# Optimization experiments

Hardware: AMD Instinct MI355X
Metric: run time of the kernel (lower is better)

The kernel has to match this reference:

```python
import jax, jax.numpy as jnp
import numpy as np

NG, NP = 40000, 80000
E = 150000
HID = 256; OUT = 256; H = 4; L = 2
D = HID // H  # 64
IN_G, IN_P = 128, 64
EDGE_DEFS = [(0, 1), (1, 0), (1, 1)]  # (src_type, dst_type): gene->peak, peak->gene, peak->peak
SCALE = 1.0 / float(np.sqrt(D))


def setup_inputs():
    key = jax.random.key(0)
    ks = iter(jax.random.split(key, 64))
    def nrm(shape, s=0.05):
        return jax.random.normal(next(ks), shape, dtype=jnp.float32) * s
    inp = {}
    inp['x_gene'] = jax.random.normal(next(ks), (NG, IN_G), dtype=jnp.float32)
    inp['x_peak'] = jax.random.normal(next(ks), (NP, IN_P), dtype=jnp.float32)
    def edges(ns, nd):
        return jnp.stack([jax.random.randint(next(ks), (E,), 0, ns),
                          jax.random.randint(next(ks), (E,), 0, nd)])
    inp['ei_gp'] = edges(NG, NP)
    inp['ei_pg'] = edges(NP, NG)
    inp['ei_pp'] = edges(NP, NP)
    # input projections per node type
    inp['W_in_g'] = nrm((IN_G, HID)); inp['b_in_g'] = jnp.zeros((HID,), jnp.float32)
    inp['W_in_p'] = nrm((IN_P, HID)); inp['b_in_p'] = jnp.zeros((HID,), jnp.float32)
    # HGTConv params, stacked over [layer, node_type] or [layer, edge_type]
    inp['Wk'] = nrm((L, 2, HID, HID)); inp['bk'] = jnp.zeros((L, 2, HID), jnp.float32)
    inp['Wq'] = nrm((L, 2, HID, HID)); inp['bq'] = jnp.zeros((L, 2, HID), jnp.float32)
    inp['Wv'] = nrm((L, 2, HID, HID)); inp['bv'] = jnp.zeros((L, 2, HID), jnp.float32)
    inp['a_rel'] = nrm((L, 3, H, D, D), 0.1)  # per-edge-type key transform
    inp['m_rel'] = nrm((L, 3, H, D, D), 0.1)  # per-edge-type message transform
    inp['p_rel'] = jnp.ones((L, 3, H), jnp.float32)  # relation prior
    inp['W_oc'] = nrm((L, 2, HID, HID)); inp['b_oc'] = jnp.zeros((L, 2, HID), jnp.float32)
    inp['skip'] = jnp.zeros((L, 2), jnp.float32)  # per-node-type skip logits
    # output projections per node type
    inp['W_out_g'] = nrm((HID, OUT)); inp['b_out_g'] = jnp.zeros((OUT,), jnp.float32)
    inp['W_out_p'] = nrm((HID, OUT)); inp['b_out_p'] = jnp.zeros((OUT,), jnp.float32)
    return inp


def _hgt_conv(xs, eis, Wk, bk, Wq, bq, Wv, bv, a_rel, m_rel, p_rel, W_oc, b_oc, skip):
    # xs: list of [N_t, HID] per node type; eis: list of [2, E] per edge type
    k = [(xs[t] @ Wk[t] + bk[t]).reshape(-1, H, D) for t in range(2)]
    q = [(xs[t] @ Wq[t] + bq[t]).reshape(-1, H, D) for t in range(2)]
    v = [(xs[t] @ Wv[t] + bv[t]).reshape(-1, H, D) for t in range(2)]
    logits = [[], []]; msgs = [[], []]; dsts = [[], []]
    for r, (st, dt) in enumerate(EDGE_DEFS):
        src, dst = eis[r][0], eis[r][1]
        k_t = jnp.einsum('nhd,hdf->nhf', k[st], a_rel[r])  # relation-specific keys at node level
        v_t = jnp.einsum('nhd,hdf->nhf', v[st], m_rel[r])  # relation-specific messages
        lg = jnp.einsum('ehd,ehd->eh', k_t[src], q[dt][dst]) * p_rel[r] * SCALE  # [E, H]
        logits[dt].append(lg); msgs[dt].append(v_t[src]); dsts[dt].append(dst)
    out = []
    for t in range(2):
        n = xs[t].shape[0]
        lg = jnp.concatenate(logits[t]); ms = jnp.concatenate(msgs[t]); dd = jnp.concatenate(dsts[t])
        # segment softmax over all incoming edges (across edge types) per dst node
        mx = jax.ops.segment_max(lg, dd, num_segments=n)            # [n, H]
        ex = jnp.exp(lg - mx[dd])
        den = jax.ops.segment_sum(ex, dd, num_segments=n)
        alpha = ex / den[dd]                                        # [Etot, H]
        agg = jax.ops.segment_sum(alpha[:, :, None] * ms, dd, num_segments=n).reshape(n, HID)
        o = jax.nn.gelu(agg) @ W_oc[t] + b_oc[t]
        a = jax.nn.sigmoid(skip[t])
        out.append(a * o + (1.0 - a) * xs[t])
    return out


def reference(x_gene, x_peak, ei_gp, ei_pg, ei_pp, W_in_g, b_in_g, W_in_p, b_in_p,
              Wk, bk, Wq, bq, Wv, bv, a_rel, m_rel, p_rel, W_oc, b_oc, skip,
              W_out_g, b_out_g, W_out_p, b_out_p):
    # eval mode: dropout disabled
    xs = [jax.nn.relu(x_gene @ W_in_g + b_in_g), jax.nn.relu(x_peak @ W_in_p + b_in_p)]
    eis = [ei_gp, ei_pg, ei_pp]
    for l in range(L):
        xs = _hgt_conv(xs, eis, Wk[l], bk[l], Wq[l], bq[l], Wv[l], bv[l],
                       a_rel[l], m_rel[l], p_rel[l], W_oc[l], b_oc[l], skip[l])
        xs = [jax.nn.relu(x) for x in xs]
    z_g = xs[0] @ W_out_g + b_out_g
    z_p = xs[1] @ W_out_p + b_out_p
    return z_g, z_p
```

## Files before the change

### kernel.cpp

```cpp
#include <hip/hip_runtime.h>

typedef unsigned short u16;
typedef unsigned int u32;
typedef __bf16 bf16x8 __attribute__((ext_vector_type(8)));
typedef float f32x4 __attribute__((ext_vector_type(4)));

#define AS_G __attribute__((address_space(1)))
#define AS_L __attribute__((address_space(3)))

__device__ __forceinline__ float b2f(u16 u){ union{u32 i; float f;}x; x.i=((u32)u)<<16; return x.f; }
__device__ __forceinline__ u16 f2b(float f){ union{float f; u32 i;}x; x.f=f; u32 r=(x.i+0x7FFFu+((x.i>>16)&1u))>>16; return (u16)r; }

__global__ void fill_f32(float* __restrict__ p, int n, float v){
  int i = blockIdx.x * 256 + threadIdx.x;
  if (i < n) p[i] = v;
}
__global__ void diag_f32(const int* __restrict__ flag, float* __restrict__ p, int n){
  if (flag[0] == 0) return;
  for (int i = blockIdx.x * 256 + threadIdx.x; i < n; i += gridDim.x * 256) p[i] = 3.0f;
}
__global__ void detect_k(const int* __restrict__ ei, int* __restrict__ mode){
  if (threadIdx.x == 0 && blockIdx.x == 0)
    mode[0] = ((ei[1] | ei[3] | ei[5] | ei[7]) == 0) ? 1 : 0;
}

__global__ void scatter_k(const int* __restrict__ ei_gp, const int* __restrict__ ei_pg,
                          const int* __restrict__ ei_pp, int E,
                          const int* __restrict__ mode,
                          int* __restrict__ cntg, int* __restrict__ cntp,
                          u32* __restrict__ slg, u32* __restrict__ slp,
                          int* __restrict__ flag)
{
  const u32 PBASE = 40000u * 768u;
  int e = blockIdx.x * 256 + threadIdx.x;
  if (e >= E) return;
  int y = blockIdx.y;
  const int* ei = (y == 0) ? ei_pg : (y == 1) ? ei_gp : ei_pp;
  int nsrc      = (y == 1) ? 40000 : 80000;
  int ndst      = (y == 0) ? 40000 : 80000;
  int* cnt      = (y == 0) ? cntg : cntp;
  u32* slots    = (y == 0) ? slg  : slp;
  int src, dst;
  if (mode[0]){ src = ei[2*(size_t)e]; dst = ei[2*(size_t)E + 2*(size_t)e]; }
  else        { src = ei[e];           dst = ei[(size_t)E + e]; }
  if ((u32)src >= (u32)nsrc || (u32)dst >= (u32)ndst){ atomicOr(flag, 1); return; }
  u32 off, rel;
  if (y == 1){ off = (u32)src * 768u + 256u;          rel = 0u; }
  else if (y == 0){ off = PBASE + (u32)src * 1280u + 256u; rel = 1u; }
  else            { off = PBASE + (u32)src * 1280u + 768u; rel = 2u; }
  int slot = atomicAdd(&cnt[dst], 1);
  if (slot < 32) slots[(size_t)dst * 32 + slot] = off | (rel << 28);
}

struct GP {
  const u16* A; int lda;
  const u16* Bt;
  const float* bias;
  const u16* xres;
  const float* skipp;
  void* C; int ldc;
  int M, K, N;
};

template<int EPI, int F32OUT>
__global__ __launch_bounds__(512)
void gemm_bt(GP p0, GP p1)
{
  const GP P = blockIdx.z ? p1 : p0;
  __shared__ __align__(16) u16 smem[24576];
  u16* Al = smem;
  u16* Bl = smem + 16384;
  const int tid  = threadIdx.x;
  const int lane = tid & 63;
  const int wid  = tid >> 6;
  const int wr   = wid >> 1, wc = wid & 1;

  const int NC = gridDim.x, NR = gridDim.y;
  const int f  = blockIdx.y * NC + blockIdx.x;
  const int NR8 = NR & ~7;
  int c, r;
  const int bulk = NC * NR8;
  if (f < bulk){
    int xcd = f & 7;
    int j = f >> 3;
    c = j % NC;
    r = (j / NC) * 8 + xcd;
  } else {
    int f2 = f - bulk;
    c = f2 % NC;
    r = NR8 + f2 / NC;
  }
  const int row0 = r * 256, col0 = c * 128;
  if (row0 >= P.M || col0 >= P.N) return;

  f32x4 acc[4][4] = {};
  const int cr  = tid >> 3;
  const int ccs = (((tid & 7) ^ (cr & 7)) * 8);

  for (int k0 = 0; k0 < P.K; k0 += 64){
    #pragma unroll
    for (int i = 0; i < 4; i++){
      int grow = row0 + i*64 + cr; grow = grow < P.M ? grow : (P.M - 1);
      const u16* g = P.A + (size_t)grow * P.lda + (k0 + ccs);
      u16* l = Al + i*4096 + wid*512;
      __builtin_amdgcn_global_load_lds((const AS_G void*)g, (AS_L void*)l, 16, 0, 0);
    }
    #pragma unroll
    for (int i = 0; i < 2; i++){
      const u16* g = P.Bt + (size_t)(col0 + i*64 + cr) * P.K + (k0 + ccs);
      u16* l = Bl + i*4096 + wid*512;
      __builtin_amdgcn_global_load_lds((const AS_G void*)g, (AS_L void*)l, 16, 0, 0);
    }
    __syncthreads();
    #pragma unroll
    for (int ks = 0; ks < 2; ks++){
      bf16x8 aF[4], bF[4];
      const int ch8 = (((ks*4 + (lane >> 4)) ^ (lane & 7))) * 8;
      #pragma unroll
      for (int m = 0; m < 4; m++)
        aF[m] = *(const bf16x8*)&Al[(size_t)(wr*64 + m*16 + (lane & 15)) * 64 + ch8];
      #pragma unroll
      for (int n = 0; n < 4; n++)
        bF[n] = *(const bf16x8*)&Bl[(size_t)(wc*64 + n*16 + (lane & 15)) * 64 + ch8];
      #pragma unroll
      for (int m = 0; m < 4; m++)
        #pragma unroll
        for (int n = 0; n < 4; n++)
          acc[m][n] = __builtin_amdgcn_mfma_f32_16x16x32_bf16(aF[m], bF[n], acc[m][n], 0, 0, 0);
    }
    __syncthreads();
  }

  float ask = 0.f;
  if (EPI == 2) ask = 1.f / (1.f + __expf(-(*P.skipp)));

  if (F32OUT){
    #pragma unroll
    for (int n = 0; n < 4; n++){
      const int col = col0 + wc*64 + n*16 + (lane & 15);
      const float bv = P.bias[col];
      #pragma unroll
      for (int m = 0; m < 4; m++){
        const int rb = row0 + wr*64 + m*16 + (lane >> 4) * 4;
        #pragma unroll
        for (int j = 0; j < 4; j++){
          int row = rb + j;
          if (row < P.M) ((float*)P.C)[(size_t)row*P.ldc + col] = acc[m][n][j] + bv;
        }
      }
    }
  } else {
    #pragma unroll
    for (int chh = 0; chh < 2; chh++){
      __syncthreads();
      if (wc == chh){
        #pragma unroll
        for (int n = 0; n < 4; n++){
          const int cl = n*16 + (lane & 15);
          const int col = col0 + chh*64 + cl;
          const float bv = P.bias[col];
          #pragma unroll
          for (int m = 0; m < 4; m++){
            const int rlb = wr*64 + m*16 + (lane >> 4) * 4;
            #pragma unroll
            for (int j = 0; j < 4; j++){
              const int rl = rlb + j;
              float v = acc[m][n][j] + bv;
              if (EPI == 1) v = fmaxf(v, 0.f);
              if (EPI == 2){
                int row = row0 + rl;
                float xr = (row < P.M) ? b2f(P.xres[(size_t)row*256 + col]) : 0.f;
                v = ask * v + (1.f - ask) * xr;
                v = fmaxf(v, 0.f);
              }
              smem[rl*72 + cl] = f2b(v);
            }
          }
        }
      }
      __syncthreads();
      #pragma unroll
      for (int t = 0; t < 4; t++){
        int idx = t*512 + tid;
        int rr2 = idx >> 3, cchunk = idx & 7;
        int grow = row0 + rr2;
        if (grow < P.M)
          *(bf16x8*)((u16*)P.C + (size_t)grow*P.ldc + col0 + chh*64 + cchunk*8) =
              *(const bf16x8*)&smem[rr2*72 + cchunk*8];
      }
    }
  }
}

__global__ void cvt_k(const float* __restrict__ in, u16* __restrict__ out, int n4){
  int i = blockIdx.x * 256 + threadIdx.x;
  if (i >= n4) return;
  float4 v = ((const float4*)in)[i];
  u16 o[4] = { f2b(v.x), f2b(v.y), f2b(v.z), f2b(v.w) };
  *(unsigned long long*)&out[(size_t)i*4] = *(unsigned long long*)o;
}

__global__ void transpose_k(const float* __restrict__ W, u16* __restrict__ Wt, int K, int N){
  int idx = blockIdx.x * 256 + threadIdx.x;
  if (idx >= K * N) return;
  int n = idx / K, k = idx % K;
  Wt[idx] = f2b(W[(size_t)k * N + n]);
}
__global__ void transpose10_k(const float* __restrict__ Wq, const float* __restrict__ Woc,
                              const float* __restrict__ Wog, const float* __restrict__ Wop,
                              u16* __restrict__ wqkv_g, u16* __restrict__ wqkv_p,
                              u16* __restrict__ woct, u16* __restrict__ woutt)
{
  int y = blockIdx.y;
  const float* W; u16* D;
  if (y < 4){ int l = y >> 1, t = y & 1;
              W = Wq + (size_t)y*65536;
              D = t ? (wqkv_p + (size_t)l*1280*256) : (wqkv_g + (size_t)l*768*256); }
  else if (y < 8){ W = Woc + (size_t)(y-4)*65536; D = woct + (size_t)(y-4)*65536; }
  else if (y == 8){ W = Wog; D = woutt; }
  else            { W = Wop; D = woutt + 65536; }
  int idx = blockIdx.x * 256 + threadIdx.x;
  int n = idx >> 8, k = idx & 255;
  D[(size_t)n*256 + k] = f2b(W[(size_t)k*256 + n]);
}

__global__ void fuse_rel_k(const float* __restrict__ Wk, const float* __restrict__ Wv,
                           const float* __restrict__ a_rel, const float* __restrict__ m_rel,
                           u16* __restrict__ wqkv_g, u16* __restrict__ wqkv_p)
{
  int y = blockIdx.y;
  int l = y / 6, rr = y % 6, rel = rr >> 1, kv = rr & 1;
  int st = (rel == 0) ? 0 : 1;
  const float* W    = (kv ? Wv : Wk) + (size_t)l*131072 + (size_t)st*65536;
  const float* arel = (kv ? m_rel : a_rel) + (size_t)l*49152 + (size_t)rel*16384;
  u16* base; size_t ld; int rowoff;
  if (rel == 0){ base = wqkv_g; ld = 768;  rowoff = 256 + kv*256; }
  else if (rel == 1){ base = wqkv_p; ld = 1280; rowoff = 256 + kv*256; }
  else              { base = wqkv_p; ld = 1280; rowoff = 768 + kv*256; }
  u16* dst = base + (size_t)l*ld*256 + (size_t)rowoff*256;
  int fo = threadIdx.x;
  int c  = blockIdx.x;
  int h = fo >> 6, f = fo & 63;
  const float* wrow = W + (size_t)c*256 + h*64;
  const float* arow = arel + (size_t)h*4096 + f;
  float s = 0.f;
  #pragma unroll 8
  for (int d = 0; d < 64; d++) s += wrow[d] * arow[(size_t)d*64];
  dst[(size_t)fo*256 + c] = f2b(s);
}

__global__ void fuse_bias_k(const float* __restrict__ bk, const float* __restrict__ bv,
                            const float* __restrict__ bq,
                            const float* __restrict__ a_rel, const float* __restrict__ m_rel,
                            float* __restrict__ bqkv_g, float* __restrict__ bqkv_p)
{
  int y = blockIdx.x, fo = threadIdx.x;
  if (y < 12){
    int l = y / 6, rr = y % 6, rel = rr >> 1, kv = rr & 1;
    int st = (rel == 0) ? 0 : 1;
    const float* b    = (kv ? bv : bk) + l*512 + st*256;
    const float* arel = (kv ? m_rel : a_rel) + (size_t)l*49152 + (size_t)rel*16384;
    float* base; int ld, rowoff;
    if (rel == 0){ base = bqkv_g; ld = 768;  rowoff = 256 + kv*256; }
    else if (rel == 1){ base = bqkv_p; ld = 1280; rowoff = 256 + kv*256; }
    else              { base = bqkv_p; ld = 1280; rowoff = 768 + kv*256; }
    int h = fo >> 6, f = fo & 63;
    float s = 0.f;
    for (int d = 0; d < 64; d++) s += b[h*64 + d] * arel[(size_t)h*4096 + (size_t)d*64 + f];
    base[(size_t)l*ld + rowoff + fo] = s;
  } else {
    int z = y - 12, l = z >> 1, t = z & 1;
    float* base = t ? bqkv_p : bqkv_g; int ld = t ? 1280 : 768;
    base[(size_t)l*ld + fo] = bq[(size_t)(l*2 + t)*256 + fo];
  }
}

__global__ __launch_bounds__(256)
void edge_agg_k(const int* __restrict__ cntg, const u32* __restrict__ slg,
                const int* __restrict__ cntp, const u32* __restrict__ slp,
                u16* qkv, const float* __restrict__ prel)
{
  const int NG = 40000;
  const size_t PBASE = (size_t)NG * 768;
  int w = blockIdx.x * 4 + (threadIdx.x >> 6);
  int lane = threadIdx.x & 63;
  const bool gene = w < NG;
  const int node = gene ? w : w - NG;
  const int* cnt = gene ? cntg : cntp;
  const u32* slots = gene ? slg : slp;

  const int h = lane >> 4;
  const int co = (h << 6) + ((lane & 15) << 2);
  const float pr0 = prel[0*4 + h] * 0.125f;
  const float pr1 = prel[1*4 + h] * 0.125f;
  const float pr2 = prel[2*4 + h] * 0.125f;

  u16* qrow = gene ? qkv + (size_t)node * 768 + co
                   : qkv + PBASE + (size_t)node * 1280 + co;
  ushort4 q4 = *(const ushort4*)qrow;
  float qv0 = b2f(q4.x), qv1 = b2f(q4.y), qv2 = b2f(q4.z), qv3 = b2f(q4.w);

  const u16* qco = qkv + co;

  float den = 0.f, ac0 = 0.f, ac1 = 0.f, ac2 = 0.f, ac3 = 0.f;

  int deg = cnt[node]; if (deg > 32) deg = 32;
  for (int i0 = 0; i0 < deg; i0 += 4){
    int c = deg - i0; c = c < 4 ? c : 4;
    ushort4 k4[4], v4[4]; float prc[4];
    #pragma unroll
    for (int j = 0; j < 4; j++){
      if (j < c){
        u32 ent = slots[(size_t)node*32 + i0 + j];
        u32 off = ent & 0x0FFFFFFFu;
        u32 rel = ent >> 28;
        const u16* base = qco + off;
        k4[j] = *(const ushort4*)base;
        v4[j] = *(const ushort4*)(base + 256);
        prc[j] = (rel == 0 ? pr0 : (rel == 1 ? pr1 : pr2));
      }
    }
    #pragma unroll
    for (int j = 0; j < 4; j++){
      if (j < c){
        float p = b2f(k4[j].x)*qv0 + b2f(k4[j].y)*qv1 + b2f(k4[j].z)*qv2 + b2f(k4[j].w)*qv3;
        p += __shfl_xor(p, 1); p += __shfl_xor(p, 2); p += __shfl_xor(p, 4); p += __shfl_xor(p, 8);
        float e = __expf(fminf(p * prc[j], 80.f));
        den += e;
        ac0 += e*b2f(v4[j].x);
        ac1 += e*b2f(v4[j].y);
        ac2 += e*b2f(v4[j].z);
        ac3 += e*b2f(v4[j].w);
      }
    }
  }
  float inv = den > 0.f ? 1.f / den : 0.f;
  float xs[4] = { ac0*inv, ac1*inv, ac2*inv, ac3*inv };
  u16 o[4];
  #pragma unroll
  for (int j = 0; j < 4; j++){
    float x = xs[j];
    float t = tanhf(0.7978845608028654f * (x + 0.044715f * x * x * x));
    o[j] = f2b(0.5f * x * (1.f + t));
  }
  *(ushort4*)qrow = *(ushort4*)o;
}

extern "C" void kernel_launch(void* const* d_in, const int* in_sizes, int n_in,
                              void* d_out, int out_size, void* d_ws, size_t ws_size,
                              hipStream_t stream)
{
  const int NG = 40000, NP = 80000, E = 150000;
  float* outF = (float*)d_out;
  const int fb = (out_size + 255) / 256;

  if (n_in != 25){ fill_f32<<<fb, 256, 0, stream>>>(outF, out_size, 2.0f); return; }
  static const int EXP[25] = {5120000,5120000,300000,300000,300000,32768,256,16384,256,
                              262144,1024,262144,1024,262144,1024,98304,98304,24,
                              262144,1024,4,65536,256,65536,256};
  bool ok = true;
  for (int i = 0; i < 25; i++){
    if (i >= 2 && i <= 4) ok = ok && (in_sizes[i] == 300000 || in_sizes[i] == 600000);
    else                  ok = ok && (in_sizes[i] == EXP[i]);
  }
  if (!ok){ fill_f32<<<fb, 256, 0, stream>>>(outF, out_size, 0.0f); return; }

  const float* x_gene = (const float*)d_in[0];
  const float* x_peak = (const float*)d_in[1];
  const int* ei_gp  = (const int*)d_in[2];
  const int* ei_pg  = (const int*)d_in[3];
  const int* ei_pp  = (const int*)d_in[4];
  const float* W_in_g = (const float*)d_in[5];  const float* b_in_g = (const float*)d_in[6];
  const float* W_in_p = (const float*)d_in[7];  const float* b_in_p = (const float*)d_in[8];
  const float* Wk     = (const float*)d_in[9];  const float* bk     = (const float*)d_in[10];
  const float* Wq     = (const float*)d_in[11]; const float* bq     = (const float*)d_in[12];
  const float* Wv     = (const float*)d_in[13]; const float* bv     = (const float*)d_in[14];
  const float* a_rel  = (const float*)d_in[15]; const float* m_rel  = (const float*)d_in[16];
  const float* p_rel  = (const float*)d_in[17];
  const float* W_oc   = (const float*)d_in[18]; const float* b_oc   = (const float*)d_in[19];
  const float* skip   = (const float*)d_in[20];
  const float* W_out_g= (const float*)d_in[21]; const float* b_out_g= (const float*)d_in[22];
  const float* W_out_p= (const float*)d_in[23]; const float* b_out_p= (const float*)d_in[24];

  char* ws = (char*)d_ws; size_t off = 0;
  auto alloc = [&](size_t nbytes) -> void* {
    void* p = ws + off; off = (off + nbytes + 255) & ~(size_t)255; return p;
  };

  u16* xg    = (u16*)alloc((size_t)NG*256*2);
  u16* xp    = (u16*)alloc((size_t)NP*256*2);
  u16* qkv   = (u16*)alloc(((size_t)NG*768 + (size_t)NP*1280)*2);
  u16* wtin_g = (u16*)alloc(256*128*2);
  u16* wtin_p = (u16*)alloc(256*64*2);
  u16* wqkv_g = (u16*)alloc((size_t)2*768*256*2);
  u16* wqkv_p = (u16*)alloc((size_t)2*1280*256*2);
  u16* woct  = (u16*)alloc((size_t)4*65536*2);
  u16* woutt = (u16*)alloc((size_t)2*65536*2);
  float* bqkv_g = (float*)alloc((size_t)2*768*4);
  float* bqkv_p = (float*)alloc((size_t)2*1280*4);
  int* cntg  = (int*)alloc((size_t)NG*4);
  int* cntp  = (int*)alloc((size_t)NP*4);
  u32* slg   = (u32*)alloc((size_t)NG*32*4);
  u32* slp   = (u32*)alloc((size_t)NP*32*4);
  int* mode  = (int*)alloc(256);
  int* flag  = (int*)alloc(256);

  if (off > ws_size){ fill_f32<<<fb, 256, 0, stream>>>(outF, out_size, 1.0f); return; }

  u16* qkvp = qkv + (size_t)NG*768;
  u16* xgb  = qkv;
  u16* xpb  = qkv + (size_t)NG*128;

  hipMemsetAsync(cntg, 0, (size_t)NG*4, stream);
  hipMemsetAsync(cntp, 0, (size_t)NP*4, stream);
  hipMemsetAsync(flag, 0, 4, stream);
  detect_k<<<1, 64, 0, stream>>>(ei_gp, mode);
  scatter_k<<<dim3((E + 255)/256, 3), 256, 0, stream>>>(ei_gp, ei_pg, ei_pp, E, mode,
                                                        cntg, cntp, slg, slp, flag);
  cvt_k<<<(NG*128/4 + 255)/256, 256, 0, stream>>>(x_gene, xgb, NG*128/4);
  cvt_k<<<(NP*64/4 + 255)/256, 256, 0, stream>>>(x_peak, xpb, NP*64/4);
  transpose_k<<<128, 256, 0, stream>>>(W_in_g, wtin_g, 128, 256);
  transpose_k<<<64,  256, 0, stream>>>(W_in_p, wtin_p, 64, 256);
  transpose10_k<<<dim3(256, 10), 256, 0, stream>>>(Wq, W_oc, W_out_g, W_out_p,
                                                   wqkv_g, wqkv_p, woct, woutt);
  fuse_rel_k<<<dim3(256, 12), 256, 0, stream>>>(Wk, Wv, a_rel, m_rel, wqkv_g, wqkv_p);
  fuse_bias_k<<<16, 256, 0, stream>>>(bk, bv, bq, a_rel, m_rel, bqkv_g, bqkv_p);

  auto mkGP = [](const u16* A, int lda, const u16* Bt, const float* bias,
                 const u16* xres, const float* skipp, void* C, int ldc,
                 int M, int K, int N) -> GP {
    GP p; p.A = A; p.lda = lda; p.Bt = Bt; p.bias = bias; p.xres = xres;
    p.skipp = skipp; p.C = C; p.ldc = ldc; p.M = M; p.K = K; p.N = N; return p;
  };

  gemm_bt<1,0><<<dim3(2, 313, 2), 512, 0, stream>>>(
      mkGP(xgb, 128, wtin_g, b_in_g, nullptr, nullptr, xg, 256, NG, 128, 256),
      mkGP(xpb,  64, wtin_p, b_in_p, nullptr, nullptr, xp, 256, NP,  64, 256));

  for (int l = 0; l < 2; l++){
    const float* pr = p_rel + l*12;
    gemm_bt<0,0><<<dim3(10, 313, 2), 512, 0, stream>>>(
        mkGP(xg, 256, wqkv_g + (size_t)l*768*256,  bqkv_g + (size_t)l*768,  nullptr, nullptr, qkv,  768,  NG, 256, 768),
        mkGP(xp, 256, wqkv_p + (size_t)l*1280*256, bqkv_p + (size_t)l*1280, nullptr, nullptr, qkvp, 1280, NP, 256, 1280));

    edge_agg_k<<<(NG + NP)/4, 256, 0, stream>>>(cntg, slg, cntp, slp, qkv, pr);

    gemm_bt<2,0><<<dim3(2, 313, 2), 512, 0, stream>>>(
        mkGP(qkv,  768,  woct + (size_t)(l*2+0)*65536, b_oc + (l*2+0)*256, xg, skip + (l*2+0), xg, 256, NG, 256, 256),
        mkGP(qkvp, 1280, woct + (size_t)(l*2+1)*65536, b_oc + (l*2+1)*256, xp, skip + (l*2+1), xp, 256, NP, 256, 256));
  }

  gemm_bt<0,1><<<dim3(2, 313, 2), 512, 0, stream>>>(
      mkGP(xg, 256, woutt,         b_out_g, nullptr, nullptr, outF,                  256, NG, 256, 256),
      mkGP(xp, 256, woutt + 65536, b_out_p, nullptr, nullptr, outF + (size_t)NG*256, 256, NP, 256, 256));

  diag_f32<<<2048, 256, 0, stream>>>(flag, outF, out_size);
}
```

Before: 853.1 us.

## Merge preprocessing kernels into one launch and widen edge gather batching

Folds the edge scatter, input bf16 conversions, weight transposes, relation-weight fusion and bias fusion into a single block-indexed prep kernel, removing seven separate launches and their serialization gaps. The edge aggregation kernel also gains a fast path for degree at most 4 and otherwise processes neighbors in batches of 8 instead of 4, so more gathers are in flight at once. The trade-off is higher register use in the aggregation kernel and hard-coded block counts tied to the problem sizes.

Measured after the change: 833.1 us. -2.3%, faster.

```diff
diff --git a/kernel.cpp b/kernel.cpp
--- a/kernel.cpp
+++ b/kernel.cpp
@@ -24,32 +24,138 @@
     mode[0] = ((ei[1] | ei[3] | ei[5] | ei[7]) == 0) ? 1 : 0;
 }
 
-__global__ void scatter_k(const int* __restrict__ ei_gp, const int* __restrict__ ei_pg,
-                          const int* __restrict__ ei_pp, int E,
-                          const int* __restrict__ mode,
-                          int* __restrict__ cntg, int* __restrict__ cntp,
-                          u32* __restrict__ slg, u32* __restrict__ slp,
-                          int* __restrict__ flag)
+struct PrepArgs {
+  const int *ei_gp, *ei_pg, *ei_pp;
+  const int* mode;
+  int *cntg, *cntp; u32 *slg, *slp; int* flag;
+  const float *x_gene, *x_peak; u16 *xgb, *xpb;
+  const float *W_in_g, *W_in_p; u16 *wtin_g, *wtin_p;
+  const float *Wq, *Woc, *Wog, *Wop;
+  u16 *wqkv_g, *wqkv_p, *woct, *woutt;
+  const float *Wk, *Wv, *a_rel, *m_rel;
+  const float *bk, *bv, *bq;
+  float *bqkv_g, *bqkv_p;
+};
+
+__global__ __launch_bounds__(256)
+void prep_k(PrepArgs A)
 {
-  const u32 PBASE = 40000u * 768u;
-  int e = blockIdx.x * 256 + threadIdx.x;
-  if (e >= E) return;
-  int y = blockIdx.y;
-  const int* ei = (y == 0) ? ei_pg : (y == 1) ? ei_gp : ei_pp;
-  int nsrc      = (y == 1) ? 40000 : 80000;
-  int ndst      = (y == 0) ? 40000 : 80000;
-  int* cnt      = (y == 0) ? cntg : cntp;
-  u32* slots    = (y == 0) ? slg  : slp;
-  int src, dst;
-  if (mode[0]){ src = ei[2*(size_t)e]; dst = ei[2*(size_t)E + 2*(size_t)e]; }
-  else        { src = ei[e];           dst = ei[(size_t)E + e]; }
-  if ((u32)src >= (u32)nsrc || (u32)dst >= (u32)ndst){ atomicOr(flag, 1); return; }
-  u32 off, rel;
-  if (y == 1){ off = (u32)src * 768u + 256u;          rel = 0u; }
-  else if (y == 0){ off = PBASE + (u32)src * 1280u + 256u; rel = 1u; }
-  else            { off = PBASE + (u32)src * 1280u + 768u; rel = 2u; }
-  int slot = atomicAdd(&cnt[dst], 1);
-  if (slot < 32) slots[(size_t)dst * 32 + slot] = off | (rel << 28);
+  const int E = 150000;
+  int bid = blockIdx.x;
+  const int tid = threadIdx.x;
+
+  if (bid < 1761){
+    int y = bid / 587;
+    int e = (bid % 587) * 256 + tid;
+    if (e >= E) return;
+    const u32 PBASE = 40000u * 768u;
+    const int* ei = (y == 0) ? A.ei_pg : (y == 1) ? A.ei_gp : A.ei_pp;
+    int nsrc = (y == 1) ? 40000 : 80000;
+    int ndst = (y == 0) ? 40000 : 80000;
+    int* cnt = (y == 0) ? A.cntg : A.cntp;
+    u32* slots = (y == 0) ? A.slg : A.slp;
+    int src, dst;
+    if (A.mode[0]){ src = ei[2*(size_t)e]; dst = ei[2*(size_t)E + 2*(size_t)e]; }
+    else          { src = ei[e];           dst = ei[(size_t)E + e]; }
+    if ((u32)src >= (u32)nsrc || (u32)dst >= (u32)ndst){ atomicOr(A.flag, 1); return; }
+    u32 off, rel;
+    if (y == 1){ off = (u32)src*768u + 256u;            rel = 0u; }
+    else if (y == 0){ off = PBASE + (u32)src*1280u + 256u; rel = 1u; }
+    else            { off = PBASE + (u32)src*1280u + 768u; rel = 2u; }
+    int slot = atomicAdd(&cnt[dst], 1);
+    if (slot < 32) slots[(size_t)dst*32 + slot] = off | (rel << 28);
+    return;
+  }
+  bid -= 1761;
+  if (bid < 5000){
+    int i = bid*256 + tid;
+    float4 v = ((const float4*)A.x_gene)[i];
+    u16 o[4] = { f2b(v.x), f2b(v.y), f2b(v.z), f2b(v.w) };
+    *(unsigned long long*)&A.xgb[(size_t)i*4] = *(unsigned long long*)o;
+    return;
+  }
+  bid -= 5000;
+  if (bid < 5000){
+    int i = bid*256 + tid;
+    float4 v = ((const float4*)A.x_peak)[i];
+    u16 o[4] = { f2b(v.x), f2b(v.y), f2b(v.z), f2b(v.w) };
+    *(unsigned long long*)&A.xpb[(size_t)i*4] = *(unsigned long long*)o;
+    return;
+  }
+  bid -= 5000;
+  if (bid < 128){
+    int idx = bid*256 + tid;
+    int n = idx / 128, k = idx % 128;
+    A.wtin_g[idx] = f2b(A.W_in_g[(size_t)k*256 + n]);
+    return;
+  }
+  bid -= 128;
+  if (bid < 64){
+    int idx = bid*256 + tid;
+    int n = idx / 64, k = idx % 64;
+    A.wtin_p[idx] = f2b(A.W_in_p[(size_t)k*256 + n]);
+    return;
+  }
+  bid -= 64;
+  if (bid < 2560){
+    int y = bid / 256;
+    const float* W; u16* D;
+    if (y < 4){ int l = y >> 1, t = y & 1;
+                W = A.Wq + (size_t)y*65536;
+                D = t ? (A.wqkv_p + (size_t)l*1280*256) : (A.wqkv_g + (size_t)l*768*256); }
+    else if (y < 8){ W = A.Woc + (size_t)(y-4)*65536; D = A.woct + (size_t)(y-4)*65536; }
+    else if (y == 8){ W = A.Wog; D = A.woutt; }
+    else            { W = A.Wop; D = A.woutt + 65536; }
+    int idx = (bid % 256) * 256 + tid;
+    int n = idx >> 8, k = idx & 255;
+    D[(size_t)n*256 + k] = f2b(W[(size_t)k*256 + n]);
+    return;
+  }
+  bid -= 2560;
+  if (bid < 3072){
+    int y = bid / 256;
+    int l = y / 6, rr = y % 6, rel = rr >> 1, kv = rr & 1;
+    int st = (rel == 0) ? 0 : 1;
+    const float* W    = (kv ? A.Wv : A.Wk) + (size_t)l*131072 + (size_t)st*65536;
+    const float* arel = (kv ? A.m_rel : A.a_rel) + (size_t)l*49152 + (size_t)rel*16384;
+    u16* base; size_t ld; int rowoff;
+    if (rel == 0){ base = A.wqkv_g; ld = 768;  rowoff = 256 + kv*256; }
+    else if (rel == 1){ base = A.wqkv_p; ld = 1280; rowoff = 256 + kv*256; }
+    else              { base = A.wqkv_p; ld = 1280; rowoff = 768 + kv*256; }
+    u16* dst = base + (size_t)l*ld*256 + (size_t)rowoff*256;
+    int fo = tid;
+    int c  = bid % 256;
+    int h = fo >> 6, f = fo & 63;
+    const float* wrow = W + (size_t)c*256 + h*64;
+    const float* arow = arel + (size_t)h*4096 + f;
+    float s = 0.f;
+    #pragma unroll 8
+    for (int d = 0; d < 64; d++) s += wrow[d] * arow[(size_t)d*64];
+    dst[(size_t)fo*256 + c] = f2b(s);
+    return;
+  }
+  bid -= 3072;
+  {
+    int y = bid, fo = tid;
+    if (y < 12){
+      int l = y / 6, rr = y % 6, rel = rr >> 1, kv = rr & 1;
+      int st = (rel == 0) ? 0 : 1;
+      const float* b    = (kv ? A.bv : A.bk) + l*512 + st*256;
+      const float* arel = (kv ? A.m_rel : A.a_rel) + (size_t)l*49152 + (size_t)rel*16384;
+      float* base; int ld, rowoff;
+      if (rel == 0){ base = A.bqkv_g; ld = 768;  rowoff = 256 + kv*256; }
+      else if (rel == 1){ base = A.bqkv_p; ld = 1280; rowoff = 256 + kv*256; }
+      else              { base = A.bqkv_p; ld = 1280; rowoff = 768 + kv*256; }
+      int h = fo >> 6, f = fo & 63;
+      float s = 0.f;
+      for (int d = 0; d < 64; d++) s += b[h*64 + d] * arel[(size_t)h*4096 + (size_t)d*64 + f];
+      base[(size_t)l*ld + rowoff + fo] = s;
+    } else {
+      int z = y - 12, l = z >> 1, t = z & 1;
+      float* base = t ? A.bqkv_p : A.bqkv_g; int ld = t ? 1280 : 768;
+      base[(size_t)l*ld + fo] = A.bq[(size_t)(l*2 + t)*256 + fo];
+    }
+  }
 }
 
 struct GP {
@@ -192,89 +298,6 @@
   }
 }
 
-__global__ void cvt_k(const float* __restrict__ in, u16* __restrict__ out, int n4){
-  int i = blockIdx.x * 256 + threadIdx.x;
-  if (i >= n4) return;
-  float4 v = ((const float4*)in)[i];
-  u16 o[4] = { f2b(v.x), f2b(v.y), f2b(v.z), f2b(v.w) };
-  *(unsigned long long*)&out[(size_t)i*4] = *(unsigned long long*)o;
-}
-
-__global__ void transpose_k(const float* __restrict__ W, u16* __restrict__ Wt, int K, int N){
-  int idx = blockIdx.x * 256 + threadIdx.x;
-  if (idx >= K * N) return;
-  int n = idx / K, k = idx % K;
-  Wt[idx] = f2b(W[(size_t)k * N + n]);
-}
-__global__ void transpose10_k(const float* __restrict__ Wq, const float* __restrict__ Woc,
-                              const float* __restrict__ Wog, const float* __restrict__ Wop,
-                              u16* __restrict__ wqkv_g, u16* __restrict__ wqkv_p,
-                              u16* __restrict__ woct, u16* __restrict__ woutt)
-{
-  int y = blockIdx.y;
-  const float* W; u16* D;
-  if (y < 4){ int l = y >> 1, t = y & 1;
-              W = Wq + (size_t)y*65536;
-              D = t ? (wqkv_p + (size_t)l*1280*256) : (wqkv_g + (size_t)l*768*256); }
-  else if (y < 8){ W = Woc + (size_t)(y-4)*65536; D = woct + (size_t)(y-4)*65536; }
-  else if (y == 8){ W = Wog; D = woutt; }
-  else            { W = Wop; D = woutt + 65536; }
-  int idx = blockIdx.x * 256 + threadIdx.x;
-  int n = idx >> 8, k = idx & 255;
-  D[(size_t)n*256 + k] = f2b(W[(size_t)k*256 + n]);
-}
-
-__global__ void fuse_rel_k(const float* __restrict__ Wk, const float* __restrict__ Wv,
-                           const float* __restrict__ a_rel, const float* __restrict__ m_rel,
-                           u16* __restrict__ wqkv_g, u16* __restrict__ wqkv_p)
-{
-  int y = blockIdx.y;
-  int l = y / 6, rr = y % 6, rel = rr >> 1, kv = rr & 1;
-  int st = (rel == 0) ? 0 : 1;
-  const float* W    = (kv ? Wv : Wk) + (size_t)l*131072 + (size_t)st*65536;
-  const float* arel = (kv ? m_rel : a_rel) + (size_t)l*49152 + (size_t)rel*16384;
-  u16* base; size_t ld; int rowoff;
-  if (rel == 0){ base = wqkv_g; ld = 768;  rowoff = 256 + kv*256; }
-  else if (rel == 1){ base = wqkv_p; ld = 1280; rowoff = 256 + kv*256; }
-  else              { base = wqkv_p; ld = 1280; rowoff = 768 + kv*256; }
-  u16* dst = base + (size_t)l*ld*256 + (size_t)rowoff*256;
-  int fo = threadIdx.x;
-  int c  = blockIdx.x;
-  int h = fo >> 6, f = fo & 63;
-  const float* wrow = W + (size_t)c*256 + h*64;
-  const float* arow = arel + (size_t)h*4096 + f;
-  float s = 0.f;
-  #pragma unroll 8
-  for (int d = 0; d < 64; d++) s += wrow[d] * arow[(size_t)d*64];
-  dst[(size_t)fo*256 + c] = f2b(s);
-}
-
-__global__ void fuse_bias_k(const float* __restrict__ bk, const float* __restrict__ bv,
-                            const float* __restrict__ bq,
-                            const float* __restrict__ a_rel, const float* __restrict__ m_rel,
-                            float* __restrict__ bqkv_g, float* __restrict__ bqkv_p)
-{
-  int y = blockIdx.x, fo = threadIdx.x;
-  if (y < 12){
-    int l = y / 6, rr = y % 6, rel = rr >> 1, kv = rr & 1;
-    int st = (rel == 0) ? 0 : 1;
-    const float* b    = (kv ? bv : bk) + l*512 + st*256;
-    const float* arel = (kv ? m_rel : a_rel) + (size_t)l*49152 + (size_t)rel*16384;
-    float* base; int ld, rowoff;
-    if (rel == 0){ base = bqkv_g; ld = 768;  rowoff = 256 + kv*256; }
-    else if (rel == 1){ base = bqkv_p; ld = 1280; rowoff = 256 + kv*256; }
-    else              { base = bqkv_p; ld = 1280; rowoff = 768 + kv*256; }
-    int h = fo >> 6, f = fo & 63;
-    float s = 0.f;
-    for (int d = 0; d < 64; d++) s += b[h*64 + d] * arel[(size_t)h*4096 + (size_t)d*64 + f];
-    base[(size_t)l*ld + rowoff + fo] = s;
-  } else {
-    int z = y - 12, l = z >> 1, t = z & 1;
-    float* base = t ? bqkv_p : bqkv_g; int ld = t ? 1280 : 768;
-    base[(size_t)l*ld + fo] = bq[(size_t)(l*2 + t)*256 + fo];
-  }
-}
-
 __global__ __launch_bounds__(256)
 void edge_agg_k(const int* __restrict__ cntg, const u32* __restrict__ slg,
                 const int* __restrict__ cntp, const u32* __restrict__ slp,
@@ -305,13 +328,12 @@
   float den = 0.f, ac0 = 0.f, ac1 = 0.f, ac2 = 0.f, ac3 = 0.f;
 
   int deg = cnt[node]; if (deg > 32) deg = 32;
-  for (int i0 = 0; i0 < deg; i0 += 4){
-    int c = deg - i0; c = c < 4 ? c : 4;
+  if (deg <= 4){
     ushort4 k4[4], v4[4]; float prc[4];
     #pragma unroll
     for (int j = 0; j < 4; j++){
-      if (j < c){
-        u32 ent = slots[(size_t)node*32 + i0 + j];
+      if (j < deg){
+        u32 ent = slots[(size_t)node*32 + j];
         u32 off = ent & 0x0FFFFFFFu;
         u32 rel = ent >> 28;
         const u16* base = qco + off;
@@ -322,7 +344,7 @@
     }
     #pragma unroll
     for (int j = 0; j < 4; j++){
-      if (j < c){
+      if (j < deg){
         float p = b2f(k4[j].x)*qv0 + b2f(k4[j].y)*qv1 + b2f(k4[j].z)*qv2 + b2f(k4[j].w)*qv3;
         p += __shfl_xor(p, 1); p += __shfl_xor(p, 2); p += __shfl_xor(p, 4); p += __shfl_xor(p, 8);
         float e = __expf(fminf(p * prc[j], 80.f));
@@ -331,6 +353,36 @@
         ac1 += e*b2f(v4[j].y);
         ac2 += e*b2f(v4[j].z);
         ac3 += e*b2f(v4[j].w);
+      }
+    }
+  } else {
+    for (int i0 = 0; i0 < deg; i0 += 8){
+      int c = deg - i0; c = c < 8 ? c : 8;
+      ushort4 k4[8], v4[8]; float prc[8];
+      #pragma unroll
+      for (int j = 0; j < 8; j++){
+        if (j < c){
+          u32 ent = slots[(size_t)node*32 + i0 + j];
+          u32 off = ent & 0x0FFFFFFFu;
+          u32 rel = ent >> 28;
+          const u16* base = qco + off;
+          k4[j] = *(const ushort4*)base;
+          v4[j] = *(const ushort4*)(base + 256);
+          prc[j] = (rel == 0 ? pr0 : (rel == 1 ? pr1 : pr2));
+        }
+      }
+      #pragma unroll
+      for (int j = 0; j < 8; j++){
+        if (j < c){
+          float p = b2f(k4[j].x)*qv0 + b2f(k4[j].y)*qv1 + b2f(k4[j].z)*qv2 + b2f(k4[j].w)*qv3;
+          p += __shfl_xor(p, 1); p += __shfl_xor(p, 2); p += __shfl_xor(p, 4); p += __shfl_xor(p, 8);
+          float e = __expf(fminf(p * prc[j], 80.f));
+          den += e;
+          ac0 += e*b2f(v4[j].x);
+          ac1 += e*b2f(v4[j].y);
+          ac2 += e*b2f(v4[j].z);
+          ac3 += e*b2f(v4[j].w);
+        }
       }
     }
   }
@@ -415,16 +467,17 @@
   hipMemsetAsync(cntp, 0, (size_t)NP*4, stream);
   hipMemsetAsync(flag, 0, 4, stream);
   detect_k<<<1, 64, 0, stream>>>(ei_gp, mode);
-  scatter_k<<<dim3((E + 255)/256, 3), 256, 0, stream>>>(ei_gp, ei_pg, ei_pp, E, mode,
-                                                        cntg, cntp, slg, slp, flag);
-  cvt_k<<<(NG*128/4 + 255)/256, 256, 0, stream>>>(x_gene, xgb, NG*128/4);
-  cvt_k<<<(NP*64/4 + 255)/256, 256, 0, stream>>>(x_peak, xpb, NP*64/4);
-  transpose_k<<<128, 256, 0, stream>>>(W_in_g, wtin_g, 128, 256);
-  transpose_k<<<64,  256, 0, stream>>>(W_in_p, wtin_p, 64, 256);
-  transpose10_k<<<dim3(256, 10), 256, 0, stream>>>(Wq, W_oc, W_out_g, W_out_p,
-                                                   wqkv_g, wqkv_p, woct, woutt);
-  fuse_rel_k<<<dim3(256, 12), 256, 0, stream>>>(Wk, Wv, a_rel, m_rel, wqkv_g, wqkv_p);
-  fuse_bias_k<<<16, 256, 0, stream>>>(bk, bv, bq, a_rel, m_rel, bqkv_g, bqkv_p);
+
+  PrepArgs PA;
+  PA.ei_gp = ei_gp; PA.ei_pg = ei_pg; PA.ei_pp = ei_pp; PA.mode = mode;
+  PA.cntg = cntg; PA.cntp = cntp; PA.slg = slg; PA.slp = slp; PA.flag = flag;
+  PA.x_gene = x_gene; PA.x_peak = x_peak; PA.xgb = xgb; PA.xpb = xpb;
+  PA.W_in_g = W_in_g; PA.W_in_p = W_in_p; PA.wtin_g = wtin_g; PA.wtin_p = wtin_p;
+  PA.Wq = Wq; PA.Woc = W_oc; PA.Wog = W_out_g; PA.Wop = W_out_p;
+  PA.wqkv_g = wqkv_g; PA.wqkv_p = wqkv_p; PA.woct = woct; PA.woutt = woutt;
+  PA.Wk = Wk; PA.Wv = Wv; PA.a_rel = a_rel; PA.m_rel = m_rel;
+  PA.bk = bk; PA.bv = bv; PA.bq = bq; PA.bqkv_g = bqkv_g; PA.bqkv_p = bqkv_p;
+  prep_k<<<17601, 256, 0, stream>>>(PA);
 
   auto mkGP = [](const u16* A, int lda, const u16* Bt, const float* bias,
                  const u16* xres, const float* skipp, void* C, int ldc,
```
